# Kernel optimization log

Hardware: AMD Instinct MI355X
Metric: run time of the kernel (lower is better)

## Reference

```python
import jax, jax.numpy as jnp
import numpy as np

N, IN_F, OUT_F, R = 8192, 4096, 4096, 16
ALPHA = 32
SCALING = ALPHA / R  # 2.0


def setup_inputs() -> dict:
    key = jax.random.key(0)
    k1, k2, k3, k4, k5 = jax.random.split(key, 5)
    return {
        "x": jax.random.normal(k1, (N, IN_F), dtype=jnp.float32),
        "W": jax.random.normal(k2, (OUT_F, IN_F), dtype=jnp.float32) * 0.02,
        "b": jax.random.normal(k3, (OUT_F,), dtype=jnp.float32) * 0.02,
        "lora_A": jax.random.normal(k4, (R, IN_F), dtype=jnp.float32) * 0.02,
        "lora_B": jax.random.normal(k5, (OUT_F, R), dtype=jnp.float32) * 0.02,
    }


def reference(x, W, b, lora_A, lora_B):
    # Base linear: x [N, in_f] @ W.T [in_f, out_f] + b -> [N, out_f]
    result = jnp.einsum('ni,oi->no', x, W) + b
    # LoRA path: (B @ (A @ x.T)).T * scaling == (x @ A.T) @ B.T * scaling
    lora = jnp.einsum('nr,or->no', jnp.einsum('ni,ri->nr', x, lora_A), lora_B)
    return result + lora * SCALING
```

## Files before the change

### kernel.cpp

```cpp
#include <hip/hip_runtime.h>
#include <hip/hip_bf16.h>
#include <stdint.h>

#define N_ROWS 8192
#define IN_F   4096
#define OUT_F  4096
#define R_LORA 16
#define KP     4160

typedef __bf16 bf16_t;
typedef __attribute__((ext_vector_type(8))) __bf16 bf16x8;
typedef __attribute__((ext_vector_type(4))) __bf16 bf16x4;
typedef __attribute__((ext_vector_type(4))) float  f32x4;
typedef __attribute__((ext_vector_type(16))) float f32x16;

__device__ __forceinline__ void load16_lds(const bf16_t* g, bf16_t* l) {
    auto gp = (const __attribute__((address_space(1))) void*)g;
    auto lp = (__attribute__((address_space(3))) void*)(uint32_t)(uintptr_t)l;
    __builtin_amdgcn_global_load_lds(gp, lp, 16, 0, 0);
}

#define PREPA_BLOCKS 2048

__global__ __launch_bounds__(256) void prep_fused(const float* __restrict__ x,
                                                  const float* __restrict__ W,
                                                  const float* __restrict__ bias,
                                                  const float* __restrict__ lA,
                                                  const float* __restrict__ lB,
                                                  bf16_t* __restrict__ Aw,
                                                  bf16_t* __restrict__ Bw) {
    int b = blockIdx.x;
    int t = threadIdx.x;
    if (b < PREPA_BLOCKS) {
        int row0 = b * 4;
        for (int rr = 0; rr < 4; ++rr) {
            int row = row0 + rr;
            const float4* xr = (const float4*)(x + (size_t)row * IN_F);
            bf16_t* ar = Aw + (size_t)row * KP;
            for (int s = t; s < 512; s += 256) {
                float4 f0 = xr[2 * s];
                float4 f1 = xr[2 * s + 1];
                bf16x8 v;
                v[0] = (bf16_t)f0.x; v[1] = (bf16_t)f0.y;
                v[2] = (bf16_t)f0.z; v[3] = (bf16_t)f0.w;
                v[4] = (bf16_t)f1.x; v[5] = (bf16_t)f1.y;
                v[6] = (bf16_t)f1.z; v[7] = (bf16_t)f1.w;
                *(bf16x8*)(ar + s * 8) = v;
            }
            if (t < 64) ar[IN_F + t] = (t == 0) ? (bf16_t)1.0f : (bf16_t)0.0f;
        }
    } else {
        int o0 = (b - PREPA_BLOCKS) * 4;
        float bl[4][R_LORA];
        for (int oo = 0; oo < 4; ++oo)
            for (int r = 0; r < R_LORA; ++r)
                bl[oo][r] = 2.0f * lB[(o0 + oo) * R_LORA + r];

        for (int j = 0; j < IN_F / (256 * 4); ++j) {
            int i4 = (j * 256 + t) * 4;
            f32x4 acc[4];
            for (int oo = 0; oo < 4; ++oo) {
                float4 w = *(const float4*)(W + (size_t)(o0 + oo) * IN_F + i4);
                acc[oo] = (f32x4){w.x, w.y, w.z, w.w};
            }
            for (int r = 0; r < R_LORA; ++r) {
                float4 a = *(const float4*)(lA + (size_t)r * IN_F + i4);
                for (int oo = 0; oo < 4; ++oo) {
                    acc[oo][0] += bl[oo][r] * a.x;
                    acc[oo][1] += bl[oo][r] * a.y;
                    acc[oo][2] += bl[oo][r] * a.z;
                    acc[oo][3] += bl[oo][r] * a.w;
                }
            }
            for (int oo = 0; oo < 4; ++oo) {
                bf16x4 v;
                v[0] = (bf16_t)acc[oo][0]; v[1] = (bf16_t)acc[oo][1];
                v[2] = (bf16_t)acc[oo][2]; v[3] = (bf16_t)acc[oo][3];
                *(bf16x4*)(Bw + (size_t)(o0 + oo) * KP + i4) = v;
            }
        }
        {
            int oo = t >> 6;
            int c  = IN_F + (t & 63);
            float v = (c == IN_F) ? bias[o0 + oo] : 0.0f;
            Bw[(size_t)(o0 + oo) * KP + c] = (bf16_t)v;
        }
    }
}

#define BM 256
#define BN 256
#define BK 64
#define NT (KP / BK)

#define VMB(n) do { asm volatile("s_waitcnt vmcnt(" #n ")" ::: "memory"); \
                    __builtin_amdgcn_s_barrier(); } while (0)

template<int Q>
__device__ __forceinline__ void phase_mma(const bf16_t* Ab, const bf16_t* Bb,
                                          f32x16 (&acc)[4][2],
                                          int rowA0, int colB0, int lhi, int l7) {
    constexpr int qa = Q & 1, qb = Q >> 1;
    bf16x8 a0[4], a1[4], bb[4];
#pragma unroll
    for (int ks = 0; ks < 4; ++ks) {
        int pos = ((((ks << 1) | lhi)) ^ l7) << 3;
        a0[ks] = *(const bf16x8*)&Ab[(qa * 128 + rowA0) * BK + pos];
        a1[ks] = *(const bf16x8*)&Ab[(qa * 128 + rowA0 + 32) * BK + pos];
        bb[ks] = *(const bf16x8*)&Bb[(qb * 128 + colB0) * BK + pos];
    }
    __builtin_amdgcn_s_setprio(1);
#pragma unroll
    for (int ks = 0; ks < 4; ++ks) {
        acc[Q][0] = __builtin_amdgcn_mfma_f32_32x32x16_bf16(a0[ks], bb[ks], acc[Q][0], 0, 0, 0);
        acc[Q][1] = __builtin_amdgcn_mfma_f32_32x32x16_bf16(a1[ks], bb[ks], acc[Q][1], 0, 0, 0);
    }
    __builtin_amdgcn_s_setprio(0);
}

__global__ __launch_bounds__(512, 2) void gemm_bt(const bf16_t* __restrict__ A,
                                                  const bf16_t* __restrict__ B,
                                                  float* __restrict__ C) {
    __shared__ __align__(16) bf16_t lds[2][2][BM * BK];

    int bid = blockIdx.x;
    int swz = (bid & 7) * 64 + (bid >> 3);
    int bm  = swz & 31;
    int bn  = swz >> 5;
    int rowBase = bm * BM;
    int colBase = bn * BN;

    const int t    = threadIdx.x;
    const int lane = t & 63;
    const int wave = t >> 6;
    const int l31  = lane & 31;
    const int lhi  = lane >> 5;
    const int l7   = lane & 7;
    const int wr   = wave >> 2;
    const int wcp  = wave & 3;
    const int rowA0 = wr * 64 + l31;
    const int colB0 = wcp * 32 + l31;

    uint32_t srcA[4], srcB[4];
#pragma unroll
    for (int s = 0; s < 4; ++s) {
        int c = s * 512 + t;
        int r = c >> 3, p = c & 7;
        uint32_t off = (uint32_t)(r * KP + ((p ^ (r & 7)) << 3));
        srcA[s] = (uint32_t)(rowBase * KP) + off;
        srcB[s] = (uint32_t)(colBase * KP) + off;
    }

    auto stageA = [&](int half, int bsel, int k0) {
#pragma unroll
        for (int s2 = 0; s2 < 2; ++s2) {
            int s = half * 2 + s2;
            load16_lds(A + srcA[s] + k0, &lds[bsel][0][(s * 512 + t) * 8]);
        }
    };
    auto stageB = [&](int half, int bsel, int k0) {
#pragma unroll
        for (int s2 = 0; s2 < 2; ++s2) {
            int s = half * 2 + s2;
            load16_lds(B + srcB[s] + k0, &lds[bsel][1][(s * 512 + t) * 8]);
        }
    };

    f32x16 acc[4][2];
#pragma unroll
    for (int q = 0; q < 4; ++q)
#pragma unroll
        for (int i = 0; i < 2; ++i)
#pragma unroll
            for (int r = 0; r < 16; ++r) acc[q][i][r] = 0.f;

    stageA(0, 0, 0);
    stageB(0, 0, 0);
    stageA(1, 0, 0);
    stageB(1, 0, 0);

    int kt = 0;
    for (; kt < NT - 1; ++kt) {
        const int bsel = kt & 1;
        const int nb   = bsel ^ 1;
        const int k1   = (kt + 1) * BK;
        const bf16_t* Ab = &lds[bsel][0][0];
        const bf16_t* Bb = &lds[bsel][1][0];

        VMB(4);
        stageA(0, nb, k1);
        phase_mma<0>(Ab, Bb, acc, rowA0, colB0, lhi, l7);
        VMB(4);
        stageB(0, nb, k1);
        phase_mma<1>(Ab, Bb, acc, rowA0, colB0, lhi, l7);
        VMB(4);
        stageA(1, nb, k1);
        phase_mma<2>(Ab, Bb, acc, rowA0, colB0, lhi, l7);
        stageB(1, nb, k1);
        phase_mma<3>(Ab, Bb, acc, rowA0, colB0, lhi, l7);
    }
    {
        const int bsel = kt & 1;
        const bf16_t* Ab = &lds[bsel][0][0];
        const bf16_t* Bb = &lds[bsel][1][0];
        VMB(4);
        phase_mma<0>(Ab, Bb, acc, rowA0, colB0, lhi, l7);
        VMB(2);
        phase_mma<1>(Ab, Bb, acc, rowA0, colB0, lhi, l7);
        VMB(0);
        phase_mma<2>(Ab, Bb, acc, rowA0, colB0, lhi, l7);
        phase_mma<3>(Ab, Bb, acc, rowA0, colB0, lhi, l7);
    }

#pragma unroll
    for (int q = 0; q < 4; ++q) {
        const int qa = q & 1, qb = q >> 1;
#pragma unroll
        for (int i = 0; i < 2; ++i) {
            int rB  = rowBase + qa * 128 + wr * 64 + i * 32 + 4 * lhi;
            int col = colBase + qb * 128 + wcp * 32 + l31;
#pragma unroll
            for (int reg = 0; reg < 16; ++reg) {
                int row = rB + (reg & 3) + 8 * (reg >> 2);
                C[(size_t)row * OUT_F + col] = acc[q][i][reg];
            }
        }
    }
}

extern "C" void kernel_launch(void* const* d_in, const int* in_sizes, int n_in,
                              void* d_out, int out_size, void* d_ws, size_t ws_size,
                              hipStream_t stream) {
    const float* x  = (const float*)d_in[0];
    const float* W  = (const float*)d_in[1];
    const float* b  = (const float*)d_in[2];
    const float* lA = (const float*)d_in[3];
    const float* lB = (const float*)d_in[4];
    float* out = (float*)d_out;

    bf16_t* Aw = (bf16_t*)d_ws;
    bf16_t* Bw = Aw + (size_t)N_ROWS * KP;

    prep_fused<<<PREPA_BLOCKS + OUT_F / 4, 256, 0, stream>>>(x, W, b, lA, lB, Aw, Bw);
    gemm_bt<<<(N_ROWS / BM) * (OUT_F / BN), 512, 0, stream>>>(Aw, Bw, out);
}
```

Measured before the change: 565.4 us.

## Give each wave a contiguous 128x64 tile and simplify the double-buffered pipeline

Each wave now owns a contiguous 128x64 output sub-tile (4 row fragments by 2 column fragments) instead of four scattered 64x32 quadrants. That cuts LDS fragment reads per K-step from 12 to 6 for the same 8 MFMAs. The four-phase interleaving of staggered A/B half-loads with per-phase waits is replaced by a simple loop: barrier, issue the whole next tile's global-to-LDS loads, wait for the current tile, then compute. The simpler schedule may hide global-load latency less finely than the staggered version and changes register pressure.

```diff
diff --git a/kernel.cpp b/kernel.cpp
--- a/kernel.cpp
+++ b/kernel.cpp
@@ -93,31 +93,6 @@
 #define BK 64
 #define NT (KP / BK)
 
-#define VMB(n) do { asm volatile("s_waitcnt vmcnt(" #n ")" ::: "memory"); \
-                    __builtin_amdgcn_s_barrier(); } while (0)
-
-template<int Q>
-__device__ __forceinline__ void phase_mma(const bf16_t* Ab, const bf16_t* Bb,
-                                          f32x16 (&acc)[4][2],
-                                          int rowA0, int colB0, int lhi, int l7) {
-    constexpr int qa = Q & 1, qb = Q >> 1;
-    bf16x8 a0[4], a1[4], bb[4];
-#pragma unroll
-    for (int ks = 0; ks < 4; ++ks) {
-        int pos = ((((ks << 1) | lhi)) ^ l7) << 3;
-        a0[ks] = *(const bf16x8*)&Ab[(qa * 128 + rowA0) * BK + pos];
-        a1[ks] = *(const bf16x8*)&Ab[(qa * 128 + rowA0 + 32) * BK + pos];
-        bb[ks] = *(const bf16x8*)&Bb[(qb * 128 + colB0) * BK + pos];
-    }
-    __builtin_amdgcn_s_setprio(1);
-#pragma unroll
-    for (int ks = 0; ks < 4; ++ks) {
-        acc[Q][0] = __builtin_amdgcn_mfma_f32_32x32x16_bf16(a0[ks], bb[ks], acc[Q][0], 0, 0, 0);
-        acc[Q][1] = __builtin_amdgcn_mfma_f32_32x32x16_bf16(a1[ks], bb[ks], acc[Q][1], 0, 0, 0);
-    }
-    __builtin_amdgcn_s_setprio(0);
-}
-
 __global__ __launch_bounds__(512, 2) void gemm_bt(const bf16_t* __restrict__ A,
                                                   const bf16_t* __restrict__ B,
                                                   float* __restrict__ C) {
@@ -137,9 +112,13 @@
     const int lhi  = lane >> 5;
     const int l7   = lane & 7;
     const int wr   = wave >> 2;
-    const int wcp  = wave & 3;
-    const int rowA0 = wr * 64 + l31;
-    const int colB0 = wcp * 32 + l31;
+    const int wc   = wave & 3;
+
+    int rowOffA[4], colOffB[2];
+#pragma unroll
+    for (int rf = 0; rf < 4; ++rf) rowOffA[rf] = (wr * 128 + rf * 32 + l31) * BK;
+#pragma unroll
+    for (int cf = 0; cf < 2; ++cf) colOffB[cf] = (wc * 64 + cf * 32 + l31) * BK;
 
     uint32_t srcA[4], srcB[4];
 #pragma unroll
@@ -151,78 +130,77 @@
         srcB[s] = (uint32_t)(colBase * KP) + off;
     }
 
-    auto stageA = [&](int half, int bsel, int k0) {
-#pragma unroll
-        for (int s2 = 0; s2 < 2; ++s2) {
-            int s = half * 2 + s2;
+    auto stage = [&](int bsel, int k0) {
+#pragma unroll
+        for (int s = 0; s < 4; ++s)
             load16_lds(A + srcA[s] + k0, &lds[bsel][0][(s * 512 + t) * 8]);
-        }
+#pragma unroll
+        for (int s = 0; s < 4; ++s)
+            load16_lds(B + srcB[s] + k0, &lds[bsel][1][(s * 512 + t) * 8]);
     };
-    auto stageB = [&](int half, int bsel, int k0) {
-#pragma unroll
-        for (int s2 = 0; s2 < 2; ++s2) {
-            int s = half * 2 + s2;
-            load16_lds(B + srcB[s] + k0, &lds[bsel][1][(s * 512 + t) * 8]);
-        }
-    };
 
     f32x16 acc[4][2];
 #pragma unroll
-    for (int q = 0; q < 4; ++q)
-#pragma unroll
-        for (int i = 0; i < 2; ++i)
-#pragma unroll
-            for (int r = 0; r < 16; ++r) acc[q][i][r] = 0.f;
-
-    stageA(0, 0, 0);
-    stageB(0, 0, 0);
-    stageA(1, 0, 0);
-    stageB(1, 0, 0);
-
-    int kt = 0;
-    for (; kt < NT - 1; ++kt) {
-        const int bsel = kt & 1;
-        const int nb   = bsel ^ 1;
-        const int k1   = (kt + 1) * BK;
-        const bf16_t* Ab = &lds[bsel][0][0];
-        const bf16_t* Bb = &lds[bsel][1][0];
-
-        VMB(4);
-        stageA(0, nb, k1);
-        phase_mma<0>(Ab, Bb, acc, rowA0, colB0, lhi, l7);
-        VMB(4);
-        stageB(0, nb, k1);
-        phase_mma<1>(Ab, Bb, acc, rowA0, colB0, lhi, l7);
-        VMB(4);
-        stageA(1, nb, k1);
-        phase_mma<2>(Ab, Bb, acc, rowA0, colB0, lhi, l7);
-        stageB(1, nb, k1);
-        phase_mma<3>(Ab, Bb, acc, rowA0, colB0, lhi, l7);
+    for (int rf = 0; rf < 4; ++rf)
+#pragma unroll
+        for (int cf = 0; cf < 2; ++cf)
+#pragma unroll
+            for (int r = 0; r < 16; ++r) acc[rf][cf][r] = 0.f;
+
+#define COMPUTE(bsel)                                                          \
+    do {                                                                       \
+        const bf16_t* Ab = &lds[bsel][0][0];                                   \
+        const bf16_t* Bb = &lds[bsel][1][0];                                   \
+        _Pragma("unroll")                                                      \
+        for (int ks = 0; ks < 4; ++ks) {                                       \
+            int pos = ((((ks << 1) | lhi)) ^ l7) << 3;                         \
+            bf16x8 af[4], bf[2];                                               \
+            _Pragma("unroll")                                                  \
+            for (int rf = 0; rf < 4; ++rf)                                     \
+                af[rf] = *(const bf16x8*)&Ab[rowOffA[rf] + pos];               \
+            _Pragma("unroll")                                                  \
+            for (int cf = 0; cf < 2; ++cf)                                     \
+                bf[cf] = *(const bf16x8*)&Bb[colOffB[cf] + pos];               \
+            __builtin_amdgcn_s_setprio(1);                                     \
+            _Pragma("unroll")                                                  \
+            for (int rf = 0; rf < 4; ++rf)                                     \
+                _Pragma("unroll")                                              \
+                for (int cf = 0; cf < 2; ++cf)                                 \
+                    acc[rf][cf] = __builtin_amdgcn_mfma_f32_32x32x16_bf16(     \
+                        af[rf], bf[cf], acc[rf][cf], 0, 0, 0);                 \
+            __builtin_amdgcn_s_setprio(0);                                     \
+        }                                                                      \
+    } while (0)
+
+    stage(0, 0);
+
+    for (int kt = 0; kt < NT - 1; ++kt) {
+        const int cur = kt & 1;
+        const int nb  = cur ^ 1;
+        __builtin_amdgcn_s_barrier();
+        stage(nb, (kt + 1) * BK);
+        asm volatile("s_waitcnt vmcnt(8)" ::: "memory");
+        __builtin_amdgcn_s_barrier();
+        COMPUTE(cur);
     }
     {
-        const int bsel = kt & 1;
-        const bf16_t* Ab = &lds[bsel][0][0];
-        const bf16_t* Bb = &lds[bsel][1][0];
-        VMB(4);
-        phase_mma<0>(Ab, Bb, acc, rowA0, colB0, lhi, l7);
-        VMB(2);
-        phase_mma<1>(Ab, Bb, acc, rowA0, colB0, lhi, l7);
-        VMB(0);
-        phase_mma<2>(Ab, Bb, acc, rowA0, colB0, lhi, l7);
-        phase_mma<3>(Ab, Bb, acc, rowA0, colB0, lhi, l7);
-    }
-
-#pragma unroll
-    for (int q = 0; q < 4; ++q) {
-        const int qa = q & 1, qb = q >> 1;
-#pragma unroll
-        for (int i = 0; i < 2; ++i) {
-            int rB  = rowBase + qa * 128 + wr * 64 + i * 32 + 4 * lhi;
-            int col = colBase + qb * 128 + wcp * 32 + l31;
+        __builtin_amdgcn_s_barrier();
+        asm volatile("s_waitcnt vmcnt(0)" ::: "memory");
+        __builtin_amdgcn_s_barrier();
+        COMPUTE(0);
+    }
+#undef COMPUTE
+
+#pragma unroll
+    for (int rf = 0; rf < 4; ++rf) {
+        int rB = rowBase + wr * 128 + rf * 32 + 4 * lhi;
+#pragma unroll
+        for (int cf = 0; cf < 2; ++cf) {
+            int col = colBase + wc * 64 + cf * 32 + l31;
 #pragma unroll
             for (int reg = 0; reg < 16; ++reg) {
                 int row = rB + (reg & 3) + 8 * (reg >> 2);
-                C[(size_t)row * OUT_F + col] = acc[q][i][reg];
+                C[(size_t)row * OUT_F + col] = acc[rf][cf][reg];
             }
         }
     }
```

Measured after the change: 538.9 us. 1.05x faster.
